# Kernel tuning notes

Measured on AMD Instinct MI355X. Metric: run time of the kernel, lower is better.

Reference implementation:

```python
import jax, jax.numpy as jnp
import numpy as np


def setup_inputs() -> dict:
    key = jax.random.key(0)
    k1, k2, k3 = jax.random.split(key, 3)
    B = 4
    NQ = 24
    dim = 2 ** NQ
    state_real = jax.random.normal(k1, (B, dim), dtype=jnp.float32)
    state_imag = jax.random.normal(k2, (B, dim), dtype=jnp.float32)
    theta = jax.random.normal(k3, (1,), dtype=jnp.float32)
    return {
        "state_real": state_real,
        "state_imag": state_imag,
        "theta": theta,
        "qubit": 5,
        "num_qubits": NQ,
    }


def reference(state_real, state_imag, theta, qubit, num_qubits):
    """Apply RX(theta) on `qubit` of a [B, 2^num_qubits] complex state (real/imag split).

    RX = [[cos(t/2), -i sin(t/2)], [-i sin(t/2), cos(t/2)]]
    qandle convention: qubit 0 is the most-significant bit, so the target-qubit
    axis sits after 2^qubit leading states.
    """
    B = state_real.shape[0]
    left = 2 ** qubit                       # states on higher-order bits
    right = 2 ** (num_qubits - qubit - 1)   # states on lower-order bits
    r = state_real.reshape(B, left, 2, right)
    im = state_imag.reshape(B, left, 2, right)
    half = theta[0] * 0.5
    c = jnp.cos(half)
    s = jnp.sin(half)
    r0, r1 = r[:, :, 0], r[:, :, 1]
    i0, i1 = im[:, :, 0], im[:, :, 1]
    # a0' = c*a0 - i*s*a1 ; a1' = c*a1 - i*s*a0
    nr0 = c * r0 + s * i1
    ni0 = c * i0 - s * r1
    nr1 = c * r1 + s * i0
    ni1 = c * i1 - s * r0
    out_r = jnp.stack([nr0, nr1], axis=2).reshape(B, -1)
    out_i = jnp.stack([ni0, ni1], axis=2).reshape(B, -1)
    return out_r, out_i
```

## Files before the change

kernel.cpp:

```cpp
#include <hip/hip_runtime.h>


typedef float f32x4 __attribute__((ext_vector_type(4)));

__global__ void __launch_bounds__(256)
rx_gate_kernel(const float* __restrict__ sr,
               const float* __restrict__ si,
               const float* __restrict__ theta,
               const int* __restrict__ qubit_p,
               const int* __restrict__ nq_p,
               float* __restrict__ out_r,
               float* __restrict__ out_i,
               long long npairs) {
    long long t = (long long)blockIdx.x * blockDim.x + threadIdx.x;
    long long p = t * 4;
    if (p >= npairs) return;

    const int shift = nq_p[0] - qubit_p[0] - 1;
    const long long right = 1ll << shift;
    const long long mask = right - 1;

    const float half = 0.5f * theta[0];
    const float c = cosf(half);
    const float s = sinf(half);

    if (((right & 3) == 0) && (p + 4 <= npairs)) {
        const long long idx0 = ((p >> shift) << (shift + 1)) | (p & mask);

        const f32x4 R0 = __builtin_nontemporal_load((const f32x4*)(sr + idx0));
        const f32x4 R1 = __builtin_nontemporal_load((const f32x4*)(sr + idx0 + right));
        const f32x4 I0 = __builtin_nontemporal_load((const f32x4*)(si + idx0));
        const f32x4 I1 = __builtin_nontemporal_load((const f32x4*)(si + idx0 + right));

        f32x4 NR0, NR1, NI0, NI1;
#pragma unroll
        for (int k = 0; k < 4; ++k) {
            NR0[k] = fmaf(c, R0[k],  s * I1[k]);
            NI0[k] = fmaf(c, I0[k], -s * R1[k]);
            NR1[k] = fmaf(c, R1[k],  s * I0[k]);
            NI1[k] = fmaf(c, I1[k], -s * R0[k]);
        }

        __builtin_nontemporal_store(NR0, (f32x4*)(out_r + idx0));
        __builtin_nontemporal_store(NR1, (f32x4*)(out_r + idx0 + right));
        __builtin_nontemporal_store(NI0, (f32x4*)(out_i + idx0));
        __builtin_nontemporal_store(NI1, (f32x4*)(out_i + idx0 + right));
    } else {
        for (int k = 0; k < 4; ++k) {
            const long long pk = p + k;
            if (pk >= npairs) break;
            const long long idx = ((pk >> shift) << (shift + 1)) | (pk & mask);
            const float r0 = sr[idx];
            const float r1 = sr[idx + right];
            const float i0 = si[idx];
            const float i1 = si[idx + right];
            out_r[idx]         = fmaf(c, r0,  s * i1);
            out_i[idx]         = fmaf(c, i0, -s * r1);
            out_r[idx + right] = fmaf(c, r1,  s * i0);
            out_i[idx + right] = fmaf(c, i1, -s * r0);
        }
    }
}

extern "C" void kernel_launch(void* const* d_in, const int* in_sizes, int n_in,
                              void* d_out, int out_size, void* d_ws, size_t ws_size,
                              hipStream_t stream) {
    const float* sr    = (const float*)d_in[0];
    const float* si    = (const float*)d_in[1];
    const float* theta = (const float*)d_in[2];
    const int* qubit_p = (const int*)d_in[3];
    const int* nq_p    = (const int*)d_in[4];

    const long long n = (long long)in_sizes[0];
    float* out_r = (float*)d_out;
    float* out_i = out_r + n;

    const long long npairs   = n / 2;
    const long long nthreads = (npairs + 3) / 4;
    const int block = 256;
    const long long grid = (nthreads + block - 1) / block;

    rx_gate_kernel<<<dim3((unsigned)grid), dim3(block), 0, stream>>>(
        sr, si, theta, qubit_p, nq_p, out_r, out_i, npairs);
}
```

Before: 189.1 us.

## Use grid-stride loop with two-way unrolled float4 processing and capped grid

Replaces the one-thread-per-four-pairs launch with a grid capped at 2048 blocks, where each thread walks a grid-stride loop handling two float4 chunks per iteration. Index math switches from 64-bit to 32-bit unsigned to cut address arithmetic. The aim is more loads in flight per thread and less per-block launch and setup overhead, while the tail is handled by a scalar remainder path. The 32-bit indexing assumes the state (n = 2^26) fits in unsigned range.

```diff
diff --git a/kernel.cpp b/kernel.cpp
--- a/kernel.cpp
+++ b/kernel.cpp
@@ -11,45 +11,98 @@
                const int* __restrict__ nq_p,
                float* __restrict__ out_r,
                float* __restrict__ out_i,
-               long long npairs) {
-    long long t = (long long)blockIdx.x * blockDim.x + threadIdx.x;
-    long long p = t * 4;
-    if (p >= npairs) return;
-
+               unsigned int npairs) {
     const int shift = nq_p[0] - qubit_p[0] - 1;
-    const long long right = 1ll << shift;
-    const long long mask = right - 1;
+    const unsigned int right = 1u << shift;
+    const unsigned int mask = right - 1u;
 
     const float half = 0.5f * theta[0];
     const float c = cosf(half);
     const float s = sinf(half);
 
-    if (((right & 3) == 0) && (p + 4 <= npairs)) {
-        const long long idx0 = ((p >> shift) << (shift + 1)) | (p & mask);
+    const unsigned int T = gridDim.x * blockDim.x;
+    const unsigned int t = blockIdx.x * blockDim.x + threadIdx.x;
 
-        const f32x4 R0 = __builtin_nontemporal_load((const f32x4*)(sr + idx0));
-        const f32x4 R1 = __builtin_nontemporal_load((const f32x4*)(sr + idx0 + right));
-        const f32x4 I0 = __builtin_nontemporal_load((const f32x4*)(si + idx0));
-        const f32x4 I1 = __builtin_nontemporal_load((const f32x4*)(si + idx0 + right));
+    if ((right & 3u) == 0) {
+        const unsigned int npb = npairs >> 2;
 
-        f32x4 NR0, NR1, NI0, NI1;
+        unsigned int pb = t;
+        for (; pb + T < npb; pb += 2u * T) {
+            const unsigned int pA = pb << 2;
+            const unsigned int pB = (pb + T) << 2;
+            const unsigned int iA = ((pA >> shift) << (shift + 1)) | (pA & mask);
+            const unsigned int iB = ((pB >> shift) << (shift + 1)) | (pB & mask);
+
+            const f32x4 R0a = __builtin_nontemporal_load((const f32x4*)(sr + iA));
+            const f32x4 R1a = __builtin_nontemporal_load((const f32x4*)(sr + iA + right));
+            const f32x4 I0a = __builtin_nontemporal_load((const f32x4*)(si + iA));
+            const f32x4 I1a = __builtin_nontemporal_load((const f32x4*)(si + iA + right));
+            const f32x4 R0b = __builtin_nontemporal_load((const f32x4*)(sr + iB));
+            const f32x4 R1b = __builtin_nontemporal_load((const f32x4*)(sr + iB + right));
+            const f32x4 I0b = __builtin_nontemporal_load((const f32x4*)(si + iB));
+            const f32x4 I1b = __builtin_nontemporal_load((const f32x4*)(si + iB + right));
+
+            f32x4 NR0a, NR1a, NI0a, NI1a, NR0b, NR1b, NI0b, NI1b;
 #pragma unroll
-        for (int k = 0; k < 4; ++k) {
-            NR0[k] = fmaf(c, R0[k],  s * I1[k]);
-            NI0[k] = fmaf(c, I0[k], -s * R1[k]);
-            NR1[k] = fmaf(c, R1[k],  s * I0[k]);
-            NI1[k] = fmaf(c, I1[k], -s * R0[k]);
+            for (int k = 0; k < 4; ++k) {
+                NR0a[k] = fmaf(c, R0a[k],  s * I1a[k]);
+                NI0a[k] = fmaf(c, I0a[k], -s * R1a[k]);
+                NR1a[k] = fmaf(c, R1a[k],  s * I0a[k]);
+                NI1a[k] = fmaf(c, I1a[k], -s * R0a[k]);
+                NR0b[k] = fmaf(c, R0b[k],  s * I1b[k]);
+                NI0b[k] = fmaf(c, I0b[k], -s * R1b[k]);
+                NR1b[k] = fmaf(c, R1b[k],  s * I0b[k]);
+                NI1b[k] = fmaf(c, I1b[k], -s * R0b[k]);
+            }
+
+            __builtin_nontemporal_store(NR0a, (f32x4*)(out_r + iA));
+            __builtin_nontemporal_store(NR1a, (f32x4*)(out_r + iA + right));
+            __builtin_nontemporal_store(NI0a, (f32x4*)(out_i + iA));
+            __builtin_nontemporal_store(NI1a, (f32x4*)(out_i + iA + right));
+            __builtin_nontemporal_store(NR0b, (f32x4*)(out_r + iB));
+            __builtin_nontemporal_store(NR1b, (f32x4*)(out_r + iB + right));
+            __builtin_nontemporal_store(NI0b, (f32x4*)(out_i + iB));
+            __builtin_nontemporal_store(NI1b, (f32x4*)(out_i + iB + right));
         }
+        for (; pb < npb; pb += T) {
+            const unsigned int p = pb << 2;
+            const unsigned int idx0 = ((p >> shift) << (shift + 1)) | (p & mask);
 
-        __builtin_nontemporal_store(NR0, (f32x4*)(out_r + idx0));
-        __builtin_nontemporal_store(NR1, (f32x4*)(out_r + idx0 + right));
-        __builtin_nontemporal_store(NI0, (f32x4*)(out_i + idx0));
-        __builtin_nontemporal_store(NI1, (f32x4*)(out_i + idx0 + right));
+            const f32x4 R0 = __builtin_nontemporal_load((const f32x4*)(sr + idx0));
+            const f32x4 R1 = __builtin_nontemporal_load((const f32x4*)(sr + idx0 + right));
+            const f32x4 I0 = __builtin_nontemporal_load((const f32x4*)(si + idx0));
+            const f32x4 I1 = __builtin_nontemporal_load((const f32x4*)(si + idx0 + right));
+
+            f32x4 NR0, NR1, NI0, NI1;
+#pragma unroll
+            for (int k = 0; k < 4; ++k) {
+                NR0[k] = fmaf(c, R0[k],  s * I1[k]);
+                NI0[k] = fmaf(c, I0[k], -s * R1[k]);
+                NR1[k] = fmaf(c, R1[k],  s * I0[k]);
+                NI1[k] = fmaf(c, I1[k], -s * R0[k]);
+            }
+
+            __builtin_nontemporal_store(NR0, (f32x4*)(out_r + idx0));
+            __builtin_nontemporal_store(NR1, (f32x4*)(out_r + idx0 + right));
+            __builtin_nontemporal_store(NI0, (f32x4*)(out_i + idx0));
+            __builtin_nontemporal_store(NI1, (f32x4*)(out_i + idx0 + right));
+        }
+        const unsigned int rem0 = npb << 2;
+        const unsigned int pk = rem0 + t;
+        if (pk < npairs) {
+            const unsigned int idx = ((pk >> shift) << (shift + 1)) | (pk & mask);
+            const float r0 = sr[idx];
+            const float r1 = sr[idx + right];
+            const float i0 = si[idx];
+            const float i1 = si[idx + right];
+            out_r[idx]         = fmaf(c, r0,  s * i1);
+            out_i[idx]         = fmaf(c, i0, -s * r1);
+            out_r[idx + right] = fmaf(c, r1,  s * i0);
+            out_i[idx + right] = fmaf(c, i1, -s * r0);
+        }
     } else {
-        for (int k = 0; k < 4; ++k) {
-            const long long pk = p + k;
-            if (pk >= npairs) break;
-            const long long idx = ((pk >> shift) << (shift + 1)) | (pk & mask);
+        for (unsigned int pk = t; pk < npairs; pk += T) {
+            const unsigned int idx = ((pk >> shift) << (shift + 1)) | (pk & mask);
             const float r0 = sr[idx];
             const float r1 = sr[idx + right];
             const float i0 = si[idx];
@@ -75,11 +128,13 @@
     float* out_r = (float*)d_out;
     float* out_i = out_r + n;
 
-    const long long npairs   = n / 2;
-    const long long nthreads = (npairs + 3) / 4;
+    const unsigned int npairs = (unsigned int)(n / 2);
+    const unsigned int npb    = npairs >> 2;
     const int block = 256;
-    const long long grid = (nthreads + block - 1) / block;
+    long long need = ((long long)npb + block - 1) / block;
+    if (need < 1) need = 1;
+    const unsigned int grid = (unsigned int)(need < 2048 ? need : 2048);
 
-    rx_gate_kernel<<<dim3((unsigned)grid), dim3(block), 0, stream>>>(
+    rx_gate_kernel<<<dim3(grid), dim3(block), 0, stream>>>(
         sr, si, theta, qubit_p, nq_p, out_r, out_i, npairs);
 }
```

New measurement: 196.4 us. 3.8% more time.
